# Kernel tuning notes

Measured on AMD Instinct MI355X. Metric: run time of the kernel, lower is better.

The kernel has to match this reference:

```python
import jax, jax.numpy as jnp
import numpy as np

N_GENE, N_CT, N_REF, N_SAMPLE = 50000, 64, 16, 1024

def setup_inputs() -> dict:
    key = jax.random.key(0)
    k1, k2, k3, k4, k5, k6 = jax.random.split(key, 6)
    x = jax.random.normal(k1, (N_GENE * N_CT * N_REF,), dtype=jnp.float32)
    idx = jax.random.randint(k2, (N_CT, N_GENE), 0, N_CT * N_GENE)
    # RefCombLayer weight: uniform around 1/n_ref
    num = 1.0 / N_REF
    w_ref = jax.random.uniform(k3, (N_REF * N_CT,), minval=num - num / 5, maxval=num + num / 5, dtype=jnp.float32)
    # CelltypeScaleLayer weight: normal(1.0, 0.1)
    w_ct = 1.0 + 0.1 * jax.random.normal(k4, (N_CT,), dtype=jnp.float32)
    # StretchLayer weight: normal(1.0, 0.1)
    w_stretch = 1.0 + 0.1 * jax.random.normal(k5, (N_GENE,), dtype=jnp.float32)
    # conv1 kernel: (n_sample, 1, n_kernel), normal(1/n_ct, 0.25/n_ct)
    conv_w = (1.0 / N_CT) + (0.25 / N_CT) * jax.random.normal(k6, (N_SAMPLE, 1, N_CT), dtype=jnp.float32)
    return {"x": x, "idx": idx, "w_ref": w_ref, "w_ct": w_ct,
            "w_stretch": w_stretch, "conv_w": conv_w,
            "N_batch": 1, "N_feature": N_GENE * N_CT}


def reference(x, idx, w_ref, w_ct, w_stretch, conv_w, N_batch, N_feature):
    # RefCombLayer: elementwise mul by per-gene-tiled ref weights
    y = x * jnp.tile(w_ref, N_GENE)                       # [n_gene*n_ct*n_ref]
    # SliceSumLayer: sum over n_ref slices
    y0 = y.reshape(N_CT * N_GENE, N_REF).sum(axis=1)      # [n_ct*n_gene]
    # CelltypeScaleLayer: gather per cell type, scale, flatten transposed
    z = y0[idx] * w_ct[:, None]                           # [n_ct, n_gene]
    y1 = z.T.reshape(-1)                                  # [n_gene*n_ct], gene-major
    # StretchLayer: per-gene weight repeated n_ct times
    y2 = y1 * jnp.repeat(w_stretch, N_CT)                 # [n_gene*n_ct]
    # Conv1d(1, n_sample, kernel=n_ct, stride=n_ct) == per-gene dot with kernel
    yk = y2.reshape(N_GENE, N_CT)                         # [n_gene, n_ct]
    out = jnp.einsum('gk,sk->sg', yk, conv_w[:, 0, :])    # [n_sample, n_gene]
    return (out, y0, y1, y2)
```

## Files before the change

### kernel.cpp

```cpp
#include <hip/hip_runtime.h>

#define NG 50000
#define NCT 64
#define NREF 16
#define NS 1024
#define N0 (NCT * NG)

#define OFF_Y0 ((size_t)NS * NG)
#define OFF_Y1 (OFF_Y0 + N0)
#define OFF_Y2 (OFF_Y1 + N0)

__global__ __launch_bounds__(256) void k_y0(const float* __restrict__ x,
                                            const float* __restrict__ w_ref,
                                            float* __restrict__ y0) {
    __shared__ float4 wl[256];
    const int tid = threadIdx.x;
    wl[tid] = reinterpret_cast<const float4*>(w_ref)[tid];
    __syncthreads();
    const int row = tid & 63;
    const float4 w0 = wl[row * 4 + 0];
    const float4 w1 = wl[row * 4 + 1];
    const float4 w2 = wl[row * 4 + 2];
    const float4 w3 = wl[row * 4 + 3];
    const float4* x4 = reinterpret_cast<const float4*>(x);
    const size_t stride = (size_t)gridDim.x * 256;
    for (size_t j = (size_t)blockIdx.x * 256 + tid; j < (size_t)N0; j += stride) {
        const float4* xp = x4 + j * 4;
        float4 a = xp[0], b = xp[1], c = xp[2], d = xp[3];
        float s = a.x * w0.x + a.y * w0.y + a.z * w0.z + a.w * w0.w
                + b.x * w1.x + b.y * w1.y + b.z * w1.z + b.w * w1.w
                + c.x * w2.x + c.y * w2.y + c.z * w2.z + c.w * w2.w
                + d.x * w3.x + d.y * w3.y + d.z * w3.z + d.w * w3.w;
        y0[j] = s;
    }
}

__global__ __launch_bounds__(256) void k_gather(const float* __restrict__ y0,
                                                const int* __restrict__ idx,
                                                const float* __restrict__ w_ct,
                                                const float* __restrict__ w_stretch,
                                                float* __restrict__ y1,
                                                float* __restrict__ y2) {
    __shared__ float T[64][65];
    const int tid = threadIdx.x;
    const int g0 = blockIdx.x * 64;
#pragma unroll
    for (int k = 0; k < 16; ++k) {
        int lin = k * 256 + tid;
        int c = lin >> 6, gl = lin & 63;
        int g = g0 + gl;
        float t = 0.f;
        if (g < NG) t = y0[idx[c * NG + g]];
        T[c][gl] = t;
    }
    __syncthreads();
#pragma unroll
    for (int k = 0; k < 16; ++k) {
        int lin = k * 256 + tid;
        int gl = lin >> 6, c = lin & 63;
        int g = g0 + gl;
        if (g < NG) {
            float t = T[c][gl];
            float v1 = t * w_ct[c];
            float v2 = v1 * w_stretch[g];
            size_t o = (size_t)g * 64 + c;
            y1[o] = v1;
            y2[o] = v2;
        }
    }
}

__global__ __launch_bounds__(256) void k_conv(const float* __restrict__ y2,
                                              const float* __restrict__ cw,
                                              float* __restrict__ out) {
    __shared__ float Yl[64 * 68];
    __shared__ float Wl[64 * 132];
    const int tid = threadIdx.x;
    const int g0 = blockIdx.x * 64;
    const int s0 = blockIdx.y * 128;

#pragma unroll
    for (int it = 0; it < 4; ++it) {
        int e0 = (it * 256 + tid) * 4;
        int gp = e0 >> 6;
        int cp = e0 & 63;
        float4 v = make_float4(0.f, 0.f, 0.f, 0.f);
        if (g0 + gp < NG) v = *reinterpret_cast<const float4*>(y2 + (size_t)(g0 + gp) * 64 + cp);
        Yl[(cp + 0) * 68 + gp] = v.x;
        Yl[(cp + 1) * 68 + gp] = v.y;
        Yl[(cp + 2) * 68 + gp] = v.z;
        Yl[(cp + 3) * 68 + gp] = v.w;
    }
#pragma unroll
    for (int it = 0; it < 8; ++it) {
        int e0 = (it * 256 + tid) * 4;
        int sp = e0 >> 6;
        int cp = e0 & 63;
        float4 v = *reinterpret_cast<const float4*>(cw + (size_t)(s0 + sp) * 64 + cp);
        Wl[(cp + 0) * 132 + sp] = v.x;
        Wl[(cp + 1) * 132 + sp] = v.y;
        Wl[(cp + 2) * 132 + sp] = v.z;
        Wl[(cp + 3) * 132 + sp] = v.w;
    }
    __syncthreads();

    const int gq4 = (tid & 15) * 4;
    const int sr = tid >> 4;
    const int sr8 = sr * 8;

    float a0[8], a1[8], a2[8], a3[8];
#pragma unroll
    for (int j = 0; j < 8; ++j) { a0[j] = a1[j] = a2[j] = a3[j] = 0.f; }

#pragma unroll 16
    for (int c = 0; c < 64; ++c) {
        float4 yv = *reinterpret_cast<const float4*>(&Yl[c * 68 + gq4]);
        float4 wA = *reinterpret_cast<const float4*>(&Wl[c * 132 + sr8]);
        float4 wB = *reinterpret_cast<const float4*>(&Wl[c * 132 + sr8 + 4]);
        float wv[8] = {wA.x, wA.y, wA.z, wA.w, wB.x, wB.y, wB.z, wB.w};
#pragma unroll
        for (int j = 0; j < 8; ++j) {
            a0[j] += yv.x * wv[j];
            a1[j] += yv.y * wv[j];
            a2[j] += yv.z * wv[j];
            a3[j] += yv.w * wv[j];
        }
    }

    const int gg = g0 + gq4;
    if (gg < NG) {
#pragma unroll
        for (int j = 0; j < 8; ++j) {
            int s = s0 + sr8 + j;
            float4 v = make_float4(a0[j], a1[j], a2[j], a3[j]);
            *reinterpret_cast<float4*>(out + (size_t)s * NG + gg) = v;
        }
    }
}

extern "C" void kernel_launch(void* const* d_in, const int* in_sizes, int n_in,
                              void* d_out, int out_size, void* d_ws, size_t ws_size,
                              hipStream_t stream) {
    const float* x         = (const float*)d_in[0];
    const int*   idx       = (const int*)d_in[1];
    const float* w_ref     = (const float*)d_in[2];
    const float* w_ct      = (const float*)d_in[3];
    const float* w_stretch = (const float*)d_in[4];
    const float* conv_w    = (const float*)d_in[5];

    float* out = (float*)d_out;
    float* y0  = out + OFF_Y0;
    float* y1  = out + OFF_Y1;
    float* y2  = out + OFF_Y2;

    k_y0<<<2048, 256, 0, stream>>>(x, w_ref, y0);
    k_gather<<<(NG + 63) / 64, 256, 0, stream>>>(y0, idx, w_ct, w_stretch, y1, y2);
    k_conv<<<dim3((NG + 63) / 64, NS / 128), 256, 0, stream>>>(y2, conv_w, out);
}
```

Before: 209.8 us.

## Compute conv GEMM with split-bf16 MFMA instead of scalar FP32 FMAs

Replaces the FP32 outer-product loop in the conv kernel with bf16 MFMA 16x16x32 instructions. Each operand is split into hi and lo bf16 parts, and three MFMAs (hi*hi, hi*lo, lo*hi) recover near-FP32 accuracy. Shared memory now holds the bf16 hi/lo pairs in a row-major, padded layout so fragments can be loaded directly. The output is still 200MB of writes, so the kernel is likely memory-bound, and the extra conversion work on load may offset the compute savings.

```diff
diff --git a/kernel.cpp b/kernel.cpp
--- a/kernel.cpp
+++ b/kernel.cpp
@@ -9,6 +9,19 @@
 #define OFF_Y0 ((size_t)NS * NG)
 #define OFF_Y1 (OFF_Y0 + N0)
 #define OFF_Y2 (OFF_Y1 + N0)
+
+typedef __attribute__((ext_vector_type(8))) short bf16x8;
+typedef __attribute__((ext_vector_type(4))) float f32x4;
+
+__device__ __forceinline__ unsigned short f2bf(float f) {
+    union { float f; unsigned u; } v; v.f = f;
+    unsigned r = v.u + 0x7fff + ((v.u >> 16) & 1);
+    return (unsigned short)(r >> 16);
+}
+__device__ __forceinline__ float bf2f(unsigned short b) {
+    union { float f; unsigned u; } v; v.u = ((unsigned)b) << 16;
+    return v.f;
+}
 
 __global__ __launch_bounds__(256) void k_y0(const float* __restrict__ x,
                                             const float* __restrict__ w_ref,
@@ -70,14 +83,17 @@
     }
 }
 
+#define STILE 128
 __global__ __launch_bounds__(256) void k_conv(const float* __restrict__ y2,
                                               const float* __restrict__ cw,
                                               float* __restrict__ out) {
-    __shared__ float Yl[64 * 68];
-    __shared__ float Wl[64 * 132];
+    __shared__ unsigned short Yhi[64 * 72];
+    __shared__ unsigned short Ylo[64 * 72];
+    __shared__ unsigned short Whi[STILE * 72];
+    __shared__ unsigned short Wlo[STILE * 72];
     const int tid = threadIdx.x;
     const int g0 = blockIdx.x * 64;
-    const int s0 = blockIdx.y * 128;
+    const int s0 = blockIdx.y * STILE;
 
 #pragma unroll
     for (int it = 0; it < 4; ++it) {
@@ -86,10 +102,13 @@
         int cp = e0 & 63;
         float4 v = make_float4(0.f, 0.f, 0.f, 0.f);
         if (g0 + gp < NG) v = *reinterpret_cast<const float4*>(y2 + (size_t)(g0 + gp) * 64 + cp);
-        Yl[(cp + 0) * 68 + gp] = v.x;
-        Yl[(cp + 1) * 68 + gp] = v.y;
-        Yl[(cp + 2) * 68 + gp] = v.z;
-        Yl[(cp + 3) * 68 + gp] = v.w;
+        unsigned short h0 = f2bf(v.x), h1 = f2bf(v.y), h2 = f2bf(v.z), h3 = f2bf(v.w);
+        int base = gp * 72 + cp;
+        Yhi[base + 0] = h0; Yhi[base + 1] = h1; Yhi[base + 2] = h2; Yhi[base + 3] = h3;
+        Ylo[base + 0] = f2bf(v.x - bf2f(h0));
+        Ylo[base + 1] = f2bf(v.y - bf2f(h1));
+        Ylo[base + 2] = f2bf(v.z - bf2f(h2));
+        Ylo[base + 3] = f2bf(v.w - bf2f(h3));
     }
 #pragma unroll
     for (int it = 0; it < 8; ++it) {
@@ -97,43 +116,70 @@
         int sp = e0 >> 6;
         int cp = e0 & 63;
         float4 v = *reinterpret_cast<const float4*>(cw + (size_t)(s0 + sp) * 64 + cp);
-        Wl[(cp + 0) * 132 + sp] = v.x;
-        Wl[(cp + 1) * 132 + sp] = v.y;
-        Wl[(cp + 2) * 132 + sp] = v.z;
-        Wl[(cp + 3) * 132 + sp] = v.w;
+        unsigned short h0 = f2bf(v.x), h1 = f2bf(v.y), h2 = f2bf(v.z), h3 = f2bf(v.w);
+        int base = sp * 72 + cp;
+        Whi[base + 0] = h0; Whi[base + 1] = h1; Whi[base + 2] = h2; Whi[base + 3] = h3;
+        Wlo[base + 0] = f2bf(v.x - bf2f(h0));
+        Wlo[base + 1] = f2bf(v.y - bf2f(h1));
+        Wlo[base + 2] = f2bf(v.z - bf2f(h2));
+        Wlo[base + 3] = f2bf(v.w - bf2f(h3));
     }
     __syncthreads();
 
-    const int gq4 = (tid & 15) * 4;
-    const int sr = tid >> 4;
-    const int sr8 = sr * 8;
-
-    float a0[8], a1[8], a2[8], a3[8];
-#pragma unroll
-    for (int j = 0; j < 8; ++j) { a0[j] = a1[j] = a2[j] = a3[j] = 0.f; }
-
-#pragma unroll 16
-    for (int c = 0; c < 64; ++c) {
-        float4 yv = *reinterpret_cast<const float4*>(&Yl[c * 68 + gq4]);
-        float4 wA = *reinterpret_cast<const float4*>(&Wl[c * 132 + sr8]);
-        float4 wB = *reinterpret_cast<const float4*>(&Wl[c * 132 + sr8 + 4]);
-        float wv[8] = {wA.x, wA.y, wA.z, wA.w, wB.x, wB.y, wB.z, wB.w};
-#pragma unroll
-        for (int j = 0; j < 8; ++j) {
-            a0[j] += yv.x * wv[j];
-            a1[j] += yv.y * wv[j];
-            a2[j] += yv.z * wv[j];
-            a3[j] += yv.w * wv[j];
-        }
-    }
-
-    const int gg = g0 + gq4;
-    if (gg < NG) {
-#pragma unroll
-        for (int j = 0; j < 8; ++j) {
-            int s = s0 + sr8 + j;
-            float4 v = make_float4(a0[j], a1[j], a2[j], a3[j]);
-            *reinterpret_cast<float4*>(out + (size_t)s * NG + gg) = v;
+    const int lane = tid & 63;
+    const int wid  = tid >> 6;
+    const int l15  = lane & 15;
+    const int l4   = lane >> 4;
+    const int nb   = wid * 32;
+
+    bf16x8 Bh[2][2], Bl[2][2];
+#pragma unroll
+    for (int n = 0; n < 2; ++n) {
+        int srow = nb + n * 16 + l15;
+#pragma unroll
+        for (int ks = 0; ks < 2; ++ks) {
+            int koff = ks * 32 + l4 * 8;
+            Bh[n][ks] = *reinterpret_cast<const bf16x8*>(&Whi[srow * 72 + koff]);
+            Bl[n][ks] = *reinterpret_cast<const bf16x8*>(&Wlo[srow * 72 + koff]);
+        }
+    }
+
+    f32x4 acc[4][2];
+#pragma unroll
+    for (int m = 0; m < 4; ++m)
+#pragma unroll
+        for (int n = 0; n < 2; ++n) acc[m][n] = (f32x4){0.f, 0.f, 0.f, 0.f};
+
+#pragma unroll
+    for (int m = 0; m < 4; ++m) {
+        int grow = m * 16 + l15;
+        bf16x8 Ah[2], Al[2];
+#pragma unroll
+        for (int ks = 0; ks < 2; ++ks) {
+            int koff = ks * 32 + l4 * 8;
+            Ah[ks] = *reinterpret_cast<const bf16x8*>(&Yhi[grow * 72 + koff]);
+            Al[ks] = *reinterpret_cast<const bf16x8*>(&Ylo[grow * 72 + koff]);
+        }
+#pragma unroll
+        for (int n = 0; n < 2; ++n) {
+#pragma unroll
+            for (int ks = 0; ks < 2; ++ks) {
+                acc[m][n] = __builtin_amdgcn_mfma_f32_16x16x32_bf16(Ah[ks], Bh[n][ks], acc[m][n], 0, 0, 0);
+                acc[m][n] = __builtin_amdgcn_mfma_f32_16x16x32_bf16(Ah[ks], Bl[n][ks], acc[m][n], 0, 0, 0);
+                acc[m][n] = __builtin_amdgcn_mfma_f32_16x16x32_bf16(Al[ks], Bh[n][ks], acc[m][n], 0, 0, 0);
+            }
+        }
+    }
+
+#pragma unroll
+    for (int m = 0; m < 4; ++m) {
+        int g4 = g0 + m * 16 + l4 * 4;
+        if (g4 < NG) {
+#pragma unroll
+            for (int n = 0; n < 2; ++n) {
+                int s = s0 + nb + n * 16 + l15;
+                *reinterpret_cast<f32x4*>(out + (size_t)s * NG + g4) = acc[m][n];
+            }
         }
     }
 }
@@ -155,5 +201,5 @@
 
     k_y0<<<2048, 256, 0, stream>>>(x, w_ref, y0);
     k_gather<<<(NG + 63) / 64, 256, 0, stream>>>(y0, idx, w_ct, w_stretch, y1, y2);
-    k_conv<<<dim3((NG + 63) / 64, NS / 128), 256, 0, stream>>>(y2, conv_w, out);
-}
+    k_conv<<<dim3((NG + 63) / 64, NS / STILE), 256, 0, stream>>>(y2, conv_w, out);
+}
```

New measurement: 184.9 us. -11.9%, faster.
